# Performance work log

Measured on AMD Instinct MI355X. Metric: run time of the kernel, lower is better.

Reference implementation:

```python
import jax, jax.numpy as jnp
import numpy as np

N = 50000      # nodes
E = 1_000_000  # edges (avg degree 20)
D = 64         # hidden dim
L = 3          # num dynamics layers
LN_EPS = 1e-5


def layernorm(h, g, b):
    mu = jnp.mean(h, axis=-1, keepdims=True)
    var = jnp.mean(jnp.square(h - mu), axis=-1, keepdims=True)
    return (h - mu) * jax.lax.rsqrt(var + LN_EPS) * g + b


def transformer_conv(h, src, dst, Wq, bq, Wk, bk, Wv, bv, Ws, bs):
    # PyG TransformerConv, heads=1, concat=False, beta=False, root_weight=True
    n = h.shape[0]
    d = Wq.shape[1]
    q = h @ Wq + bq            # [N, D] queries (dst side)
    k = h @ Wk + bk            # [N, D] keys   (src side)
    v = h @ Wv + bv            # [N, D] values (src side)
    logits = jnp.sum(q[dst] * k[src], axis=-1) / jnp.sqrt(jnp.asarray(d, h.dtype))  # [E]
    # segment softmax over incoming edges of each dst node
    m = jax.ops.segment_max(logits, dst, num_segments=n)      # [N]
    e = jnp.exp(logits - m[dst])                               # [E]
    s = jax.ops.segment_sum(e, dst, num_segments=n)            # [N]
    a = e / s[dst]                                             # [E]
    agg = jax.ops.segment_sum(a[:, None] * v[src], dst, num_segments=n)  # [N, D]
    return agg + h @ Ws + bs   # root/skip connection


def setup_inputs() -> dict:
    key = jax.random.key(0)
    ks = jax.random.split(key, 24)
    w = lambda k, shape: (jax.random.normal(k, shape, jnp.float32) * 0.05)
    inp = {
        "x": jax.random.normal(ks[0], (N, D), jnp.float32),
        "edge_index": jax.random.randint(ks[1], (2, E), 0, N, jnp.int32),
        # input_proj conv params
        "Wq0": w(ks[2], (D, D)), "bq0": w(ks[3], (D,)),
        "Wk0": w(ks[4], (D, D)), "bk0": w(ks[5], (D,)),
        "Wv0": w(ks[6], (D, D)), "bv0": w(ks[7], (D,)),
        "Ws0": w(ks[8], (D, D)), "bs0": w(ks[9], (D,)),
        "ln0_g": jnp.ones((D,), jnp.float32), "ln0_b": jnp.zeros((D,), jnp.float32),
        # stacked dynamics conv params [L, ...]
        "Wq": w(ks[10], (L, D, D)), "bq": w(ks[11], (L, D)),
        "Wk": w(ks[12], (L, D, D)), "bk": w(ks[13], (L, D)),
        "Wv": w(ks[14], (L, D, D)), "bv": w(ks[15], (L, D)),
        "Ws": w(ks[16], (L, D, D)), "bs": w(ks[17], (L, D)),
        "ln_g": jnp.ones((L, D), jnp.float32), "ln_b": jnp.zeros((L, D), jnp.float32),
    }
    return inp


def reference(x, edge_index, Wq0, bq0, Wk0, bk0, Wv0, bv0, Ws0, bs0, ln0_g, ln0_b,
              Wq, bq, Wk, bk, Wv, bv, Ws, bs, ln_g, ln_b):
    src, dst = edge_index[0], edge_index[1]
    h = transformer_conv(x, src, dst, Wq0, bq0, Wk0, bk0, Wv0, bv0, Ws0, bs0)
    h = jax.nn.relu(layernorm(h, ln0_g, ln0_b))
    # dropout is identity in eval mode
    for i in range(L):
        hi = transformer_conv(h, src, dst, Wq[i], bq[i], Wk[i], bk[i],
                              Wv[i], bv[i], Ws[i], bs[i])
        h = jax.nn.relu(layernorm(hi + h, ln_g[i], ln_b[i]))
    return h
```

## Files before the change

kernel.cpp:

```cpp
#include <hip/hip_runtime.h>
#include <math.h>


#define DD 64
#define NB_HIST 128
#define CHUNK_SHIFT 13

typedef __attribute__((ext_vector_type(8))) _Float16 h8;
typedef __attribute__((ext_vector_type(2))) _Float16 h2;
typedef __attribute__((ext_vector_type(4))) float f32x4;
typedef __attribute__((ext_vector_type(2))) float f32x2;

#define QSCALE 0.18033688f

__device__ __forceinline__ unsigned short f2h(float f) {
    union { _Float16 h; unsigned short u; } c;
    c.h = (_Float16)f;
    return c.u;
}
__device__ __forceinline__ h2 u2h2(unsigned u) {
    union { unsigned u; h2 h; } c; c.u = u; return c.h;
}
__device__ __forceinline__ unsigned pk2u(float a, float b) {
    union { decltype(__builtin_amdgcn_cvt_pkrtz(0.f, 0.f)) h; unsigned u; } c;
    c.h = __builtin_amdgcn_cvt_pkrtz(a, b);
    return c.u;
}

__global__ __launch_bounds__(1024) void hist_prep(
    const int* __restrict__ dst, unsigned* __restrict__ cb,
    unsigned short* __restrict__ rank, int E, int nbw,
    const float* __restrict__ x, unsigned short* __restrict__ hbf, int nD,
    const float* __restrict__ W0, const float* __restrict__ W1,
    const float* __restrict__ W2, const float* __restrict__ W3,
    const float* __restrict__ Wqs, const float* __restrict__ Wks,
    const float* __restrict__ Wvs, const float* __restrict__ Wss,
    unsigned short* __restrict__ Wt) {
    extern __shared__ unsigned hist[];
    int blk = blockIdx.x;
    for (int w = threadIdx.x; w < nbw; w += blockDim.x) hist[w] = 0;
    __syncthreads();
    int beg = blk << CHUNK_SHIFT;
    int end = min(E, beg + (1 << CHUNK_SHIFT));
    for (int e = beg + (int)threadIdx.x; e < end; e += blockDim.x) {
        int d = dst[e];
        unsigned sh = (unsigned)(d & 1) * 16u;
        unsigned old = atomicAdd(&hist[d >> 1], 1u << sh);
        rank[e] = (unsigned short)((old >> sh) & 0xffffu);
    }
    __syncthreads();
    unsigned* out = cb + (size_t)blk * nbw;
    for (int w = threadIdx.x; w < nbw; w += blockDim.x) out[w] = hist[w];

    int total = nD + 16 * 4096;
    int stride = gridDim.x * blockDim.x;
    for (int i = blk * blockDim.x + threadIdx.x; i < total; i += stride) {
        if (i < nD) { hbf[i] = f2h(x[i]); continue; }
        int id = i - nD;
        int mat = id >> 12, rem = id & 4095;
        int nn = rem >> 6, kk = rem & 63;
        int layer = mat >> 2, wh = mat & 3;
        const float* W;
        if (layer == 0) W = wh == 0 ? W0 : wh == 1 ? W1 : wh == 2 ? W2 : W3;
        else {
            const float* base = wh == 0 ? Wqs : wh == 1 ? Wks : wh == 2 ? Wvs : Wss;
            W = base + (size_t)(layer - 1) * 4096;
        }
        float val = W[kk * 64 + nn];
        if (wh == 0) val *= QSCALE;
        Wt[id] = f2h(val);
    }
}

__global__ __launch_bounds__(256) void prefix_blk(unsigned* __restrict__ cb,
                                                  int* __restrict__ counts,
                                                  int nbw, int n) {
    int w = blockIdx.x * blockDim.x + threadIdx.x;
    if (w >= nbw) return;
    unsigned acc = 0;
#pragma unroll 1
    for (int c = 0; c < NB_HIST; c += 16) {
        unsigned t[16];
#pragma unroll
        for (int j = 0; j < 16; ++j) t[j] = cb[(size_t)(c + j) * nbw + w];
#pragma unroll
        for (int j = 0; j < 16; ++j) {
            unsigned v = t[j];
            cb[(size_t)(c + j) * nbw + w] = acc;
            acc += v;
        }
    }
    counts[2 * w] = (int)(acc & 0xffffu);
    int b1 = 2 * w + 1;
    if (b1 < n) counts[b1] = (int)(acc >> 16);
}

__global__ __launch_bounds__(1024) void scan_local(const int* __restrict__ counts,
                                                   int* __restrict__ localscan,
                                                   int* __restrict__ blockSums, int n) {
    __shared__ int sh[1024];
    int i = blockIdx.x * 1024 + threadIdx.x;
    int val = (i < n) ? counts[i] : 0;
    sh[threadIdx.x] = val;
    __syncthreads();
    for (int off = 1; off < 1024; off <<= 1) {
        int t = (threadIdx.x >= off) ? sh[threadIdx.x - off] : 0;
        __syncthreads();
        sh[threadIdx.x] += t;
        __syncthreads();
    }
    if (i < n) localscan[i] = sh[threadIdx.x] - val;
    if (threadIdx.x == 1023) blockSums[blockIdx.x] = sh[1023];
}

__global__ __launch_bounds__(64) void scan_tops(int* __restrict__ blockSums, int nb) {
    int i = threadIdx.x;
    int val = (i < nb) ? blockSums[i] : 0;
    int s = val;
#pragma unroll
    for (int off = 1; off < 64; off <<= 1) {
        int t = __shfl_up(s, off, 64);
        if (i >= off) s += t;
    }
    if (i < nb) blockSums[i] = s - val;
}

__global__ void emit_rowptr(const int* __restrict__ localscan,
                            const int* __restrict__ blockSums,
                            int* __restrict__ row_ptr, int n, int E) {
    int i = blockIdx.x * blockDim.x + threadIdx.x;
    if (i < n) row_ptr[i] = localscan[i] + blockSums[i >> 10];
    if (i == 0) row_ptr[n] = E;
}

__global__ __launch_bounds__(256) void scatter3(const int* __restrict__ src,
                                                const int* __restrict__ dst,
                                                const unsigned* __restrict__ cb,
                                                const unsigned short* __restrict__ rank,
                                                const int* __restrict__ row_ptr,
                                                int* __restrict__ col, int E, int nbw) {
    int e = blockIdx.x * blockDim.x + threadIdx.x;
    if (e >= E) return;
    int d = dst[e];
    int blk = e >> CHUNK_SHIFT;
    unsigned sh = (unsigned)(d & 1) * 16u;
    unsigned pre = (cb[(size_t)blk * nbw + (d >> 1)] >> sh) & 0xffffu;
    int slot = row_ptr[d] + (int)pre + (int)rank[e];
    __builtin_nontemporal_store(src[e] << 7, &col[slot]);
}

__global__ __launch_bounds__(256) void gemm_mfma(
    const unsigned short* __restrict__ hbf, const unsigned short* __restrict__ Wt,
    const float* __restrict__ Bq, const float* __restrict__ Bk,
    const float* __restrict__ Bv, const float* __restrict__ Bs,
    int with_res,
    unsigned short* __restrict__ qO, unsigned char* __restrict__ kvO,
    unsigned short* __restrict__ sO, int ntiles) {
    int lane = threadIdx.x & 63;
    int wave = threadIdx.x >> 6;
    int ml = lane & 15, ql = lane >> 4;

    const unsigned short* W = Wt + wave * 4096;
    h8 wfrag[4][2];
#pragma unroll
    for (int t = 0; t < 4; ++t)
#pragma unroll
        for (int kh = 0; kh < 2; ++kh)
            wfrag[t][kh] = *(const h8*)(W + (t * 16 + ml) * 64 + kh * 32 + ql * 8);

    const float* bias = wave == 0 ? Bq : wave == 1 ? Bk : wave == 2 ? Bv : Bs;
    float4 bias4[4];
#pragma unroll
    for (int t = 0; t < 4; ++t) {
        bias4[t] = *(const float4*)(bias + t * 16 + ql * 4);
        if (wave == 0) {
            bias4[t].x *= QSCALE; bias4[t].y *= QSCALE;
            bias4[t].z *= QSCALE; bias4[t].w *= QSCALE;
        }
    }

    for (int tile = blockIdx.x; tile < ntiles; tile += gridDim.x) {
        int node0 = tile * 16;
        h8 hfrag[2];
#pragma unroll
        for (int kh = 0; kh < 2; ++kh)
            hfrag[kh] = *(const h8*)(hbf + (size_t)(node0 + ml) * 64 + kh * 32 + ql * 8);
        f32x4 acc[4];
#pragma unroll
        for (int t = 0; t < 4; ++t) {
            acc[t][0] = bias4[t].x; acc[t][1] = bias4[t].y;
            acc[t][2] = bias4[t].z; acc[t][3] = bias4[t].w;
        }
#pragma unroll
        for (int t = 0; t < 4; ++t)
#pragma unroll
            for (int kh = 0; kh < 2; ++kh)
                acc[t] = __builtin_amdgcn_mfma_f32_16x16x32_f16(
                    wfrag[t][kh], hfrag[kh], acc[t], 0, 0, 0);

        size_t rowe = (size_t)(node0 + ml) * 64;
        if (wave == 0) {
#pragma unroll
            for (int t = 0; t < 4; ++t) {
                uint2 st;
                st.x = pk2u(acc[t][0], acc[t][1]);
                st.y = pk2u(acc[t][2], acc[t][3]);
                *(uint2*)(qO + rowe + t * 16 + ql * 4) = st;
            }
        } else if (wave == 3) {
#pragma unroll
            for (int t = 0; t < 4; ++t) {
                float4 st = {acc[t][0], acc[t][1], acc[t][2], acc[t][3]};
                if (with_res) {
                    uint2 hv = *(const uint2*)(hbf + rowe + t * 16 + ql * 4);
                    h2 r0 = u2h2(hv.x), r1 = u2h2(hv.y);
                    st.x += (float)r0[0]; st.y += (float)r0[1];
                    st.z += (float)r1[0]; st.w += (float)r1[1];
                }
                uint2 sp;
                sp.x = pk2u(st.x, st.y);
                sp.y = pk2u(st.z, st.w);
                *(uint2*)(sO + rowe + t * 16 + ql * 4) = sp;
            }
        } else {
            size_t kvr = (size_t)(node0 + ml) * 128 + (wave == 2 ? 8 : 0);
#pragma unroll
            for (int t = 0; t < 4; ++t) {
                int pk = __builtin_amdgcn_cvt_pk_fp8_f32(acc[t][0], acc[t][1], 0, false);
                pk = __builtin_amdgcn_cvt_pk_fp8_f32(acc[t][2], acc[t][3], pk, true);
                size_t addr = kvr + (size_t)(t * 2 + (ql >> 1)) * 16 + (ql & 1) * 4;
                *(unsigned*)(kvO + addr) = (unsigned)pk;
            }
        }
    }
}

#define EDGE_COMP(U) do {                                                      \
    f32x2 k0 = __builtin_amdgcn_cvt_pk_f32_fp8((U).x, false);                  \
    f32x2 k1 = __builtin_amdgcn_cvt_pk_f32_fp8((U).x, true);                   \
    f32x2 k2 = __builtin_amdgcn_cvt_pk_f32_fp8((U).y, false);                  \
    f32x2 k3 = __builtin_amdgcn_cvt_pk_f32_fp8((U).y, true);                   \
    float d = qf0 * k0[0];                                                     \
    d = fmaf(qf1, k0[1], d); d = fmaf(qf2, k1[0], d); d = fmaf(qf3, k1[1], d); \
    d = fmaf(qf4, k2[0], d); d = fmaf(qf5, k2[1], d); d = fmaf(qf6, k3[0], d); \
    d = fmaf(qf7, k3[1], d);                                                   \
    d += __shfl_xor(d, 1); d += __shfl_xor(d, 2); d += __shfl_xor(d, 4);       \
    float p = exp2f(d); ssum += p;                                             \
    f32x2 w0 = __builtin_amdgcn_cvt_pk_f32_fp8((U).z, false);                  \
    f32x2 w1 = __builtin_amdgcn_cvt_pk_f32_fp8((U).z, true);                   \
    f32x2 w2 = __builtin_amdgcn_cvt_pk_f32_fp8((U).w, false);                  \
    f32x2 w3 = __builtin_amdgcn_cvt_pk_f32_fp8((U).w, true);                   \
    aa.x = fmaf(w0[0], p, aa.x); aa.y = fmaf(w0[1], p, aa.y);                  \
    aa.z = fmaf(w1[0], p, aa.z); aa.w = fmaf(w1[1], p, aa.w);                  \
    ab.x = fmaf(w2[0], p, ab.x); ab.y = fmaf(w2[1], p, ab.y);                  \
    ab.z = fmaf(w3[0], p, ab.z); ab.w = fmaf(w3[1], p, ab.w);                  \
} while (0)

__global__ __launch_bounds__(256) void attn_agg_ln(
    const unsigned short* __restrict__ qh, const unsigned char* __restrict__ kv,
    const unsigned short* __restrict__ sk,
    const int* __restrict__ row_ptr, const int* __restrict__ col,
    const float* __restrict__ g, const float* __restrict__ b,
    float* __restrict__ out, unsigned short* __restrict__ hbf_out, int n) {
    int node = blockIdx.x * 4 + (threadIdx.x >> 6);
    int lane = threadIdx.x & 63;
    if (node >= n) return;
    int grp = lane >> 3;
    int qi = lane & 7;

    size_t ro = (size_t)node * DD + qi * 8;
    uint4 qu = *(const uint4*)(qh + ro);
    uint4 su = *(const uint4*)(sk + ro);
    int beg = row_ptr[node], end = row_ptr[node + 1];

    h2 q0 = u2h2(qu.x), q1 = u2h2(qu.y), q2 = u2h2(qu.z), q3 = u2h2(qu.w);
    float qf0 = (float)q0[0], qf1 = (float)q0[1], qf2 = (float)q1[0], qf3 = (float)q1[1];
    float qf4 = (float)q2[0], qf5 = (float)q2[1], qf6 = (float)q3[0], qf7 = (float)q3[1];

    float ssum = 0.0f;
    float4 aa = {0.f, 0.f, 0.f, 0.f}, ab = {0.f, 0.f, 0.f, 0.f};

    int e = beg + grp;
    int cv0 = (e < end) ? col[e] : -1;
    int cv1 = (e + 8 < end) ? col[e + 8] : -1;
    for (int e0 = beg; e0 < end; e0 += 16) {
        bool a0 = cv0 >= 0, a1 = cv1 >= 0;
        uint4 u0, u1;
        if (a0) u0 = *(const uint4*)(kv + cv0 + qi * 16);
        if (a1) u1 = *(const uint4*)(kv + cv1 + qi * 16);
        e += 16;
        cv0 = (e < end) ? col[e] : -1;
        cv1 = (e + 8 < end) ? col[e + 8] : -1;
        if (a0) EDGE_COMP(u0);
        if (a1) EDGE_COMP(u1);
    }

#pragma unroll
    for (int off = 8; off <= 32; off <<= 1) {
        ssum += __shfl_xor(ssum, off);
        aa.x += __shfl_xor(aa.x, off); aa.y += __shfl_xor(aa.y, off);
        aa.z += __shfl_xor(aa.z, off); aa.w += __shfl_xor(aa.w, off);
        ab.x += __shfl_xor(ab.x, off); ab.y += __shfl_xor(ab.y, off);
        ab.z += __shfl_xor(ab.z, off); ab.w += __shfl_xor(ab.w, off);
    }
    float inv = (end > beg) ? 1.0f / ssum : 0.0f;
    aa.x *= inv; aa.y *= inv; aa.z *= inv; aa.w *= inv;
    ab.x *= inv; ab.y *= inv; ab.z *= inv; ab.w *= inv;

    {
        h2 t0 = u2h2(su.x), t1 = u2h2(su.y), t2 = u2h2(su.z), t3 = u2h2(su.w);
        aa.x += (float)t0[0]; aa.y += (float)t0[1];
        aa.z += (float)t1[0]; aa.w += (float)t1[1];
        ab.x += (float)t2[0]; ab.y += (float)t2[1];
        ab.z += (float)t3[0]; ab.w += (float)t3[1];
    }

    float s1 = aa.x + aa.y + aa.z + aa.w + ab.x + ab.y + ab.z + ab.w;
    s1 += __shfl_xor(s1, 1);
    s1 += __shfl_xor(s1, 2);
    s1 += __shfl_xor(s1, 4);
    float mu = s1 * (1.0f / DD);
    float dx0 = aa.x - mu, dx1 = aa.y - mu, dx2 = aa.z - mu, dx3 = aa.w - mu;
    float dx4 = ab.x - mu, dx5 = ab.y - mu, dx6 = ab.z - mu, dx7 = ab.w - mu;
    float s2v = dx0 * dx0 + dx1 * dx1 + dx2 * dx2 + dx3 * dx3
              + dx4 * dx4 + dx5 * dx5 + dx6 * dx6 + dx7 * dx7;
    s2v += __shfl_xor(s2v, 1);
    s2v += __shfl_xor(s2v, 2);
    s2v += __shfl_xor(s2v, 4);
    float var = s2v * (1.0f / DD);
    float is = rsqrtf(var + 1e-5f);
    float4 g4a = *(const float4*)(g + qi * 8);
    float4 g4b = *(const float4*)(g + qi * 8 + 4);
    float4 b4a = *(const float4*)(b + qi * 8);
    float4 b4b = *(const float4*)(b + qi * 8 + 4);
    float4 ya, yb;
    ya.x = fmaxf(dx0 * is * g4a.x + b4a.x, 0.0f);
    ya.y = fmaxf(dx1 * is * g4a.y + b4a.y, 0.0f);
    ya.z = fmaxf(dx2 * is * g4a.z + b4a.z, 0.0f);
    ya.w = fmaxf(dx3 * is * g4a.w + b4a.w, 0.0f);
    yb.x = fmaxf(dx4 * is * g4b.x + b4b.x, 0.0f);
    yb.y = fmaxf(dx5 * is * g4b.y + b4b.y, 0.0f);
    yb.z = fmaxf(dx6 * is * g4b.z + b4b.z, 0.0f);
    yb.w = fmaxf(dx7 * is * g4b.w + b4b.w, 0.0f);
    if (grp == 0) {
        if (out) {
            *(float4*)(out + ro) = ya;
            *(float4*)(out + ro + 4) = yb;
        }
        uint4 hv;
        hv.x = pk2u(ya.x, ya.y);
        hv.y = pk2u(ya.z, ya.w);
        hv.z = pk2u(yb.x, yb.y);
        hv.w = pk2u(yb.z, yb.w);
        *(uint4*)(hbf_out + ro) = hv;
    }
}

extern "C" void kernel_launch(void* const* d_in, const int* in_sizes, int n_in,
                              void* d_out, int out_size, void* d_ws, size_t ws_size,
                              hipStream_t stream) {
    const int D = DD;
    const float* x = (const float*)d_in[0];
    const int n = in_sizes[0] / D;
    const int* ei = (const int*)d_in[1];
    const int E = in_sizes[1] / 2;
    const int* srcp = ei;
    const int* dstp = ei + E;
    const int nbw = (n + 1) / 2;

    static bool s_attr = false;
    if (!s_attr) {
        s_attr = true;
        (void)hipFuncSetAttribute((const void*)hist_prep,
                                  hipFuncAttributeMaxDynamicSharedMemorySize, 102400);
    }

    char* wsp = (char*)d_ws;
    auto take = [&](size_t bytes) {
        char* p = wsp;
        wsp += (bytes + 255) & ~(size_t)255;
        return (void*)p;
    };
    int* counts    = (int*)take((size_t)n * 4);
    int* row_ptr   = (int*)take((size_t)(n + 1) * 4);
    unsigned* cb   = (unsigned*)take((size_t)NB_HIST * nbw * 4);
    unsigned short* rankb = (unsigned short*)take((size_t)E * 2);
    int* col       = (int*)take((size_t)E * 4);
    int* localscan = (int*)take((size_t)n * 4);
    int* blockSums = (int*)take((size_t)1024 * 4);
    size_t fsz = (size_t)n * D * 4;
    unsigned short* qb  = (unsigned short*)take(fsz / 2);
    unsigned char* kvb  = (unsigned char*)take(fsz / 2);
    unsigned short* sb  = (unsigned short*)take(fsz / 2);
    unsigned short* hbf = (unsigned short*)take(fsz / 2);
    unsigned short* Wt  = (unsigned short*)take((size_t)16 * 4096 * 2);

    int tb = 256;
    size_t ldsH = (size_t)nbw * 4;
    int nbScan = (n + 1023) / 1024;
    hist_prep<<<NB_HIST, 1024, ldsH, stream>>>(
        dstp, cb, rankb, E, nbw,
        x, hbf, n * D,
        (const float*)d_in[2], (const float*)d_in[4], (const float*)d_in[6],
        (const float*)d_in[8], (const float*)d_in[12], (const float*)d_in[14],
        (const float*)d_in[16], (const float*)d_in[18], Wt);
    prefix_blk<<<(nbw + tb - 1) / tb, tb, 0, stream>>>(cb, counts, nbw, n);
    scan_local<<<nbScan, 1024, 0, stream>>>(counts, localscan, blockSums, n);
    scan_tops<<<1, 64, 0, stream>>>(blockSums, nbScan);
    emit_rowptr<<<(n + tb - 1) / tb, tb, 0, stream>>>(localscan, blockSums, row_ptr, n, E);
    scatter3<<<(E + tb - 1) / tb, tb, 0, stream>>>(srcp, dstp, cb, rankb,
                                                   row_ptr, col, E, nbw);

    int ntiles = n / 16;
    int nba = (n + 3) / 4;
    for (int layer = 0; layer < 4; ++layer) {
        const float *bq_, *bk_, *bv_, *bs_, *g_, *b_;
        if (layer == 0) {
            bq_ = (const float*)d_in[3];  bk_ = (const float*)d_in[5];
            bv_ = (const float*)d_in[7];  bs_ = (const float*)d_in[9];
            g_  = (const float*)d_in[10]; b_  = (const float*)d_in[11];
        } else {
            int i = layer - 1;
            bq_ = (const float*)d_in[13] + (size_t)i * D;
            bk_ = (const float*)d_in[15] + (size_t)i * D;
            bv_ = (const float*)d_in[17] + (size_t)i * D;
            bs_ = (const float*)d_in[19] + (size_t)i * D;
            g_  = (const float*)d_in[20] + (size_t)i * D;
            b_  = (const float*)d_in[21] + (size_t)i * D;
        }
        gemm_mfma<<<512, 256, 0, stream>>>(hbf, Wt + (size_t)layer * 4 * 4096,
                                           bq_, bk_, bv_, bs_,
                                           layer == 0 ? 0 : 1,
                                           qb, kvb, sb, ntiles);
        attn_agg_ln<<<nba, 256, 0, stream>>>(qb, kvb, sb, row_ptr, col, g_, b_,
                                             layer == 3 ? (float*)d_out : nullptr,
                                             hbf, n);
    }
}
```

Before: 356.1 us.

## Replace random CSR scatter with two-pass bucketed scatter for locality

The single random-write scatter that builds the CSR column array is replaced by two passes. The first pass buckets each edge's (slot, src) record by destination slot range, using shared-memory counters and global bucket cursors. The second pass writes each bucket into col, so writes land within a localized 8K-entry window. This aims to cut scattered-write traffic, but it adds an 8-byte-per-edge intermediate buffer, one extra kernel launch and atomic contention.

```diff
diff --git a/kernel.cpp b/kernel.cpp
--- a/kernel.cpp
+++ b/kernel.cpp
@@ -127,26 +127,71 @@
 
 __global__ void emit_rowptr(const int* __restrict__ localscan,
                             const int* __restrict__ blockSums,
-                            int* __restrict__ row_ptr, int n, int E) {
+                            int* __restrict__ row_ptr,
+                            unsigned* __restrict__ gcur, int n, int E) {
     int i = blockIdx.x * blockDim.x + threadIdx.x;
     if (i < n) row_ptr[i] = localscan[i] + blockSums[i >> 10];
     if (i == 0) row_ptr[n] = E;
-}
-
-__global__ __launch_bounds__(256) void scatter3(const int* __restrict__ src,
-                                                const int* __restrict__ dst,
-                                                const unsigned* __restrict__ cb,
-                                                const unsigned short* __restrict__ rank,
-                                                const int* __restrict__ row_ptr,
-                                                int* __restrict__ col, int E, int nbw) {
-    int e = blockIdx.x * blockDim.x + threadIdx.x;
-    if (e >= E) return;
-    int d = dst[e];
-    int blk = e >> CHUNK_SHIFT;
-    unsigned sh = (unsigned)(d & 1) * 16u;
-    unsigned pre = (cb[(size_t)blk * nbw + (d >> 1)] >> sh) & 0xffffu;
-    int slot = row_ptr[d] + (int)pre + (int)rank[e];
-    __builtin_nontemporal_store(src[e] << 7, &col[slot]);
+    if (i < 128) gcur[i] = (unsigned)(i << CHUNK_SHIFT);
+}
+
+__global__ __launch_bounds__(1024) void bucketA(
+    const int* __restrict__ src, const int* __restrict__ dst,
+    const unsigned* __restrict__ cb, const unsigned short* __restrict__ rank,
+    const int* __restrict__ row_ptr, unsigned* __restrict__ gcur,
+    uint2* __restrict__ rec, int E, int nbw) {
+    __shared__ unsigned cnt[128];
+    __shared__ unsigned base[128];
+    int tid = threadIdx.x;
+    if (tid < 128) cnt[tid] = 0;
+    __syncthreads();
+    int beg = blockIdx.x << CHUNK_SHIFT;
+    int slotv[8], srcv[8], bv[8];
+#pragma unroll
+    for (int j = 0; j < 8; ++j) {
+        int e = beg + tid + (j << 10);
+        bv[j] = -1;
+        if (e < E) {
+            int d = dst[e];
+            unsigned sh = (unsigned)(d & 1) * 16u;
+            unsigned pre = (cb[(size_t)blockIdx.x * nbw + (d >> 1)] >> sh) & 0xffffu;
+            int slot = row_ptr[d] + (int)pre + (int)rank[e];
+            slotv[j] = slot;
+            srcv[j] = src[e] << 7;
+            int b = slot >> CHUNK_SHIFT;
+            bv[j] = b;
+            atomicAdd(&cnt[b], 1u);
+        }
+    }
+    __syncthreads();
+    if (tid < 128) {
+        unsigned c = cnt[tid];
+        base[tid] = c ? atomicAdd(&gcur[tid], c) : 0u;
+        cnt[tid] = 0;
+    }
+    __syncthreads();
+#pragma unroll
+    for (int j = 0; j < 8; ++j) {
+        if (bv[j] >= 0) {
+            unsigned p = base[bv[j]] + atomicAdd(&cnt[bv[j]], 1u);
+            uint2 r; r.x = (unsigned)slotv[j]; r.y = (unsigned)srcv[j];
+            rec[p] = r;
+        }
+    }
+}
+
+__global__ __launch_bounds__(1024) void bucketB(const uint2* __restrict__ rec,
+                                                int* __restrict__ col, int E) {
+    int i = (blockIdx.x << CHUNK_SHIFT) + threadIdx.x;
+#pragma unroll
+    for (int j = 0; j < 8; ++j) {
+        if (i < E) {
+            uint2 r = rec[i];
+            if (r.x < (unsigned)E)
+                col[r.x] = (int)r.y;
+        }
+        i += 1024;
+    }
 }
 
 __global__ __launch_bounds__(256) void gemm_mfma(
@@ -367,6 +412,7 @@
     const int* srcp = ei;
     const int* dstp = ei + E;
     const int nbw = (n + 1) / 2;
+    const int nchunk = (E + (1 << CHUNK_SHIFT) - 1) >> CHUNK_SHIFT;
 
     static bool s_attr = false;
     if (!s_attr) {
@@ -385,6 +431,8 @@
     int* row_ptr   = (int*)take((size_t)(n + 1) * 4);
     unsigned* cb   = (unsigned*)take((size_t)NB_HIST * nbw * 4);
     unsigned short* rankb = (unsigned short*)take((size_t)E * 2);
+    unsigned* gcur = (unsigned*)take((size_t)128 * 4);
+    uint2* rec     = (uint2*)take((size_t)E * 8);
     int* col       = (int*)take((size_t)E * 4);
     int* localscan = (int*)take((size_t)n * 4);
     int* blockSums = (int*)take((size_t)1024 * 4);
@@ -407,9 +455,11 @@
     prefix_blk<<<(nbw + tb - 1) / tb, tb, 0, stream>>>(cb, counts, nbw, n);
     scan_local<<<nbScan, 1024, 0, stream>>>(counts, localscan, blockSums, n);
     scan_tops<<<1, 64, 0, stream>>>(blockSums, nbScan);
-    emit_rowptr<<<(n + tb - 1) / tb, tb, 0, stream>>>(localscan, blockSums, row_ptr, n, E);
-    scatter3<<<(E + tb - 1) / tb, tb, 0, stream>>>(srcp, dstp, cb, rankb,
-                                                   row_ptr, col, E, nbw);
+    emit_rowptr<<<(n + tb - 1) / tb, tb, 0, stream>>>(localscan, blockSums,
+                                                      row_ptr, gcur, n, E);
+    bucketA<<<nchunk, 1024, 0, stream>>>(srcp, dstp, cb, rankb, row_ptr,
+                                         gcur, rec, E, nbw);
+    bucketB<<<nchunk, 1024, 0, stream>>>(rec, col, E);
 
     int ntiles = n / 16;
     int nba = (n + 3) / 4;
```

New measurement: 360.0 us. About the same (+1.1%).
